# Performance work log

Hardware: AMD Instinct MI355X
Metric: run time of the kernel (lower is better)

## Reference

```python
import jax, jax.numpy as jnp
import numpy as np

D = 512      # input_dim == encoder d_model
E = 512      # embedding_dim (codebook dim)
V = 8192     # num_embeddings
NC = 1       # num_codebooks
L = 6        # encoder layers
H = 8        # heads
F = 2048     # ffn dim
HD = D // H
EPS = 1e-5


def layernorm(x, s, b):
    m = jnp.mean(x, -1, keepdims=True)
    v = jnp.mean((x - m) ** 2, -1, keepdims=True)
    return (x - m) * jax.lax.rsqrt(v + EPS) * s + b


def sinusoidal_pe(T):
    pos = np.arange(T, dtype=np.float32)[:, None]
    i = np.arange(0, D, 2, dtype=np.float32)[None, :]
    ang = pos / np.power(10000.0, i / D)
    pe = np.zeros((T, D), np.float32)
    pe[:, 0::2] = np.sin(ang)
    pe[:, 1::2] = np.cos(ang)
    return jnp.asarray(pe)


def setup_inputs():
    key = jax.random.key(0)
    ks = jax.random.split(key, 12)
    B, T = 8, 1024
    xs = jax.random.normal(ks[0], (B, T, D), jnp.float32)
    xs_lens = (T // 2 + jax.random.randint(ks[1], (B,), 0, T // 2)).astype(jnp.int32)
    mask_indices = jax.random.uniform(ks[2], (B, T)) < 0.12  # span-mask surrogate
    sc = lambda k, shape, s=0.02: jax.random.normal(k, shape, jnp.float32) * s
    return {
        "xs": xs, "xs_lens": xs_lens, "mask_indices": mask_indices,
        "W_embed": sc(ks[3], (D, D), D ** -0.5),
        "ln1_s": jnp.ones((L, D)), "ln1_b": jnp.zeros((L, D)),
        "Wqkv": sc(ks[4], (L, D, 3 * D)), "Wo": sc(ks[5], (L, D, D)),
        "ln2_s": jnp.ones((L, D)), "ln2_b": jnp.zeros((L, D)),
        "W1": sc(ks[6], (L, D, F)), "W2": sc(ks[7], (L, F, D)),
        "an_s": jnp.ones((D,)), "an_b": jnp.zeros((D,)),
        "iln_s": jnp.ones((D,)), "iln_b": jnp.zeros((D,)),
        "mask_emb": sc(ks[8], (D,), 0.1),
        "top_n_out": sc(ks[9], (NC, D, V)),
        "projection": sc(ks[10], (D, E), (2.0 / (D + E)) ** 0.5),  # xavier_normal, frozen
        "embeddings": jax.random.normal(ks[11], (NC, E, V), jnp.float32),  # frozen codebook
    }


def encoder_blocks(x, pad_mask, ln1_s, ln1_b, Wqkv, Wo, ln2_s, ln2_b, W1, W2, an_s, an_b):
    B, T, _ = x.shape
    attn_bias = jnp.where(pad_mask, 0.0, -1e9)[:, None, None, :]  # [B,1,1,T]

    def layer(x, p):
        l1s, l1b, wqkv, wo, l2s, l2b, w1, w2 = p
        h = layernorm(x, l1s, l1b)
        q, k, v = jnp.split(h @ wqkv, 3, axis=-1)
        q = q.reshape(B, T, H, HD)
        k = k.reshape(B, T, H, HD)
        v = v.reshape(B, T, H, HD)
        scores = jnp.einsum('bqhd,bkhd->bhqk', q, k) * (HD ** -0.5) + attn_bias
        o = jnp.einsum('bhqk,bkhd->bqhd', jax.nn.softmax(scores, axis=-1), v)
        x = x + o.reshape(B, T, D) @ wo
        h = layernorm(x, l2s, l2b)
        x = x + jax.nn.relu(h @ w1) @ w2
        return x, None

    x, _ = jax.lax.scan(layer, x, (ln1_s, ln1_b, Wqkv, Wo, ln2_s, ln2_b, W1, W2))
    return layernorm(x, an_s, an_b)


def nearest_ids(x, iln_s, iln_b, projection, embeddings):
    # layernorm -> projection -> squared-distance argmin per codebook
    B, T, _ = x.shape
    z = layernorm(x, iln_s, iln_b) @ projection        # [B,T,E]
    flat = z.reshape(-1, E)                            # [N,E]
    d = (jnp.sum(flat ** 2, 1)[None, :, None]
         + jnp.sum(embeddings ** 2, 1)[:, None, :]
         - 2.0 * jnp.einsum('ne,gev->gnv', flat, embeddings))  # [NC,N,V]
    return jnp.argmin(d, -1).T.reshape(B, T, NC)


def reference(xs, xs_lens, mask_indices, W_embed, ln1_s, ln1_b, Wqkv, Wo, ln2_s, ln2_b,
              W1, W2, an_s, an_b, iln_s, iln_b, mask_emb, top_n_out, projection, embeddings):
    B, T, _ = xs.shape
    pad_mask = jnp.arange(T)[None, :] < xs_lens[:, None]              # [B,T]
    x = xs @ W_embed + sinusoidal_pe(T)[None]                         # encoder.embed
    target_ids = nearest_ids(x, iln_s, iln_b, projection, embeddings)  # [B,T,NC]
    masked_xs = jnp.where(mask_indices[..., None], mask_emb, x)
    out = encoder_blocks(masked_xs, pad_mask, ln1_s, ln1_b, Wqkv, Wo,
                         ln2_s, ln2_b, W1, W2, an_s, an_b)            # [B,T,D]
    logits = jnp.einsum('btd,gdv->bgtv', out, top_n_out)              # [B,NC,T,V]
    lsm = jax.nn.log_softmax(logits, axis=-1)
    tgt = jnp.transpose(target_ids, (0, 2, 1))                        # [B,NC,T]
    ent = -jnp.take_along_axis(lsm, tgt[..., None], axis=-1)[..., 0]  # [B,NC,T]
    m = (pad_mask & mask_indices).astype(jnp.float32)                 # [B,T]
    loss = jnp.sum(ent * m[:, None, :]) / (jnp.sum(m) * NC)
    return loss
```

## Files before the change

kernel.cpp:

```cpp
#include <hip/hip_runtime.h>
#include <hip/hip_bf16.h>

#define D_ 512
#define T_ 1024
#define B_ 8
#define H_ 8
#define F_ 2048
#define V_ 8192
#define L_ 6
#define NTOK 8192
#define EPS_ 1e-5f
#define NCAP 2048

typedef short short8 __attribute__((ext_vector_type(8)));
typedef float floatx4 __attribute__((ext_vector_type(4)));

__device__ __forceinline__ float bf2f(unsigned short u) {
  union { unsigned int i; float f; } v; v.i = ((unsigned int)u) << 16; return v.f;
}
__device__ __forceinline__ unsigned short f2bf(float f) {
  unsigned int u = __float_as_uint(f);
  return (unsigned short)((u + 0x7fffu + ((u >> 16) & 1u)) >> 16);
}
__device__ __forceinline__ float ldf(const void* p, long long i, int bf) {
  if (bf) return bf2f(((const unsigned short*)p)[i]);
  return ((const float*)p)[i];
}
__device__ __forceinline__ void ld16(const unsigned short* g, unsigned short* l) {
  __builtin_amdgcn_global_load_lds(
      (const __attribute__((address_space(1))) unsigned int*)g,
      (__attribute__((address_space(3))) unsigned int*)l, 16, 0, 0);
}
__device__ __forceinline__ unsigned int fkey(float f) {
  unsigned int u = __float_as_uint(f);
  return (u & 0x80000000u) ? ~u : (u ^ 0x80000000u);
}

__global__ void detect_kernel(const unsigned int* xsw, const unsigned int* mw, int* flags) {
  __shared__ int cnt[256];
  __shared__ int m01[256], mlo[256], mhi[256];
  int tid = threadIdx.x;
  int c = 0;
  for (int t = tid; t < 1024; t += 256) {
    unsigned int lo = xsw[t] & 0xffffu;
    int ok;
    if (lo == 0u) ok = 1;
    else { unsigned int e = (lo >> 7) & 0xffu; ok = (e >= 90u && e <= 140u); }
    c += ok;
  }
  int n01 = 0, lo38 = 0, hi38 = 0;
  for (int t = tid; t < 2048; t += 256) {
    unsigned int w = mw[t];
    if (w > 1u) n01 = 1;
    if ((w & 0xffffu) == 0x3f80u) lo38 = 1;
    if ((w >> 16) == 0x3f80u) hi38 = 1;
  }
  cnt[tid] = c; m01[tid] = n01; mlo[tid] = lo38; mhi[tid] = hi38;
  __syncthreads();
  for (int s = 128; s > 0; s >>= 1) {
    if (tid < s) {
      cnt[tid] += cnt[tid + s];
      m01[tid] |= m01[tid + s]; mlo[tid] |= mlo[tid + s]; mhi[tid] |= mhi[tid + s];
    }
    __syncthreads();
  }
  if (tid == 0) {
    flags[0] = (cnt[0] > 700) ? 1 : 0;
    int fmt;
    if (!m01[0]) fmt = 0;
    else if (mlo[0]) fmt = 2;
    else if (mhi[0]) fmt = 3;
    else fmt = 1;
    flags[1] = fmt;
  }
}

__global__ void conv_all_kernel(const void* d4, const void* d5, const void* d8,
                                const void* d9, const void* d12, const void* d13,
                                const void* d14, const void* d15, const void* d16,
                                float* P, const int* flags) {
  int i = blockIdx.x * 256 + threadIdx.x;
  if (i >= 14848) return;
  int bf = flags[0];
  const void* src; int off;
  if (i < 3072) { src = d4; off = 0; }
  else if (i < 6144) { src = d5; off = 3072; }
  else if (i < 9216) { src = d8; off = 6144; }
  else if (i < 12288) { src = d9; off = 9216; }
  else if (i < 12800) { src = d12; off = 12288; }
  else if (i < 13312) { src = d13; off = 12800; }
  else if (i < 13824) { src = d14; off = 13312; }
  else if (i < 14336) { src = d15; off = 13824; }
  else { src = d16; off = 14336; }
  P[i] = ldf(src, i - off, bf);
}

__global__ void convb_kernel(const void* src, unsigned short* dst, int n, const int* flags) {
  int i = blockIdx.x * 256 + threadIdx.x;
  if (i < n) {
    if (flags[0]) dst[i] = ((const unsigned short*)src)[i];
    else dst[i] = f2bf(((const float*)src)[i]);
  }
}

__global__ __launch_bounds__(256) void trans_kernel(const void* src, unsigned short* dst,
                                                    int K, int N, const int* flags) {
  int bf = flags[0];
  __shared__ unsigned short tile[32][33];
  int n0 = blockIdx.x * 32, k0 = blockIdx.y * 32, batch = blockIdx.z;
  long long sbase = (long long)batch * K * N;
  long long dbase = (long long)batch * N * K;
  int c = threadIdx.x & 31, r8 = threadIdx.x >> 5;
#pragma unroll
  for (int rr = 0; rr < 4; ++rr) {
    int r = r8 + rr * 8;
    tile[r][c] = f2bf(ldf(src, sbase + (long long)(k0 + r) * N + n0 + c, bf));
  }
  __syncthreads();
#pragma unroll
  for (int rr = 0; rr < 4; ++rr) {
    int nn = r8 + rr * 8;
    dst[dbase + (long long)(n0 + nn) * K + k0 + c] = tile[c][nn];
  }
}

__global__ __launch_bounds__(256) void trans_big_kernel(const void* top, const void* emb,
                                                        unsigned short* TOPT, unsigned short* EMBT,
                                                        float* en, const int* flags) {
  int bf = flags[0];
  __shared__ unsigned short tile[32][33];
  int n0 = blockIdx.x * 32, k0 = blockIdx.y * 32, z = blockIdx.z;
  const void* src = z ? emb : top;
  unsigned short* dst = z ? EMBT : TOPT;
  int c = threadIdx.x & 31, r8 = threadIdx.x >> 5;
#pragma unroll
  for (int rr = 0; rr < 4; ++rr) {
    int r = r8 + rr * 8;
    tile[r][c] = f2bf(ldf(src, (long long)(k0 + r) * V_ + n0 + c, bf));
  }
  __syncthreads();
#pragma unroll
  for (int rr = 0; rr < 4; ++rr) {
    int nn = r8 + rr * 8;
    dst[(long long)(n0 + nn) * D_ + k0 + c] = tile[c][nn];
  }
  if (z == 1 && threadIdx.x < 32) {
    int nn = threadIdx.x;
    float s = 0.f;
#pragma unroll
    for (int r = 0; r < 32; ++r) { float x = bf2f(tile[r][nn]); s += x * x; }
    atomicAdd(&en[n0 + nn], s);
  }
}

__global__ void prep_kernel(const void* mask, const int* lens, int* maski, float* mcomb,
                            int* idx, int* cnt, const int* flags) {
  int i = blockIdx.x * 256 + threadIdx.x;
  if (i >= NTOK) return;
  int fmt = flags[1];
  int mi;
  if (fmt == 0) mi = ((const int*)mask)[i] != 0;
  else if (fmt == 1) mi = ((const unsigned char*)mask)[i] != 0;
  else if (fmt == 2) mi = ((const unsigned short*)mask)[i] != 0;
  else mi = ((const float*)mask)[i] != 0.f;
  int b = i >> 10, t = i & (T_ - 1);
  int act = mi && (t < lens[b]);
  maski[i] = mi;
  mcomb[i] = act ? 1.f : 0.f;
  if (act) {
    int p = atomicAdd(cnt, 1);
    if (p < NCAP) idx[p] = i;
  }
}

#define BK 32

template<int BN>
__device__ __forceinline__ void stage_tile(const unsigned short* A, long long ga0, long long ga1,
                                           const unsigned short* BT, long long gb0, long long gb1,
                                           int k0, unsigned short (*Ab)[BK],
                                           unsigned short (*Bb)[BK], int wave, int c16) {
  ld16(A + ga0 + k0 + c16 * 8, &Ab[wave * 32][0]);
  ld16(A + ga1 + k0 + c16 * 8, &Ab[wave * 32 + 16][0]);
  if constexpr (BN == 128) {
    ld16(BT + gb0 + k0 + c16 * 8, &Bb[wave * 32][0]);
    ld16(BT + gb1 + k0 + c16 * 8, &Bb[wave * 32 + 16][0]);
  } else {
    ld16(BT + gb0 + k0 + c16 * 8, &Bb[wave * 16][0]);
  }
}

template<int BN>
__device__ __forceinline__ void mfma_pipe(const unsigned short* A, long long ga0, long long ga1,
                                          const unsigned short* BT, int n0, int Kdim,
                                          unsigned short (*As)[BK], unsigned short (*Bs)[BK],
                                          floatx4 (*acc)[BN / 32], int tid) {
  constexpr int NB = BN / 32;
  int wave = tid >> 6, lane = tid & 63;
  int r16 = lane >> 2, c16 = lane & 3;
  int lrow = lane & 15, quad = lane >> 4;
  int wm = (wave & 1) * 64, wn = (wave >> 1) * (BN / 2);
  int NT = Kdim / BK;
  long long gb0, gb1 = 0;
  if constexpr (BN == 128) {
    gb0 = (long long)(n0 + wave * 32 + r16) * Kdim;
    gb1 = gb0 + 16LL * Kdim;
  } else {
    gb0 = (long long)(n0 + wave * 16 + r16) * Kdim;
  }
  stage_tile<BN>(A, ga0, ga1, BT, gb0, gb1, 0, As, Bs, wave, c16);
  stage_tile<BN>(A, ga0, ga1, BT, gb0, gb1, BK, As + 128, Bs + BN, wave, c16);
  int cur = 0, nxt = 2;
  for (int t = 0; t < NT; ++t) {
    if (t == NT - 1) {
      asm volatile("s_waitcnt vmcnt(0)" ::: "memory");
    } else {
      if constexpr (BN == 128) asm volatile("s_waitcnt vmcnt(4)" ::: "memory");
      else                     asm volatile("s_waitcnt vmcnt(3)" ::: "memory");
    }
    __builtin_amdgcn_s_barrier();
    if (t + 2 < NT)
      stage_tile<BN>(A, ga0, ga1, BT, gb0, gb1, (t + 2) * BK,
                     As + nxt * 128, Bs + nxt * BN, wave, c16);
    unsigned short (*Ac)[BK] = As + cur * 128;
    unsigned short (*Bc)[BK] = Bs + cur * BN;
    short8 af[4], bfr[NB];
#pragma unroll
    for (int i = 0; i < 4; ++i) af[i] = *(const short8*)&Ac[wm + i * 16 + lrow][quad * 8];
#pragma unroll
    for (int j = 0; j < NB; ++j) bfr[j] = *(const short8*)&Bc[wn + j * 16 + lrow][quad * 8];
#pragma unroll
    for (int i = 0; i < 4; ++i)
#pragma unroll
      for (int j = 0; j < NB; ++j)
        acc[i][j] = __builtin_amdgcn_mfma_f32_16x16x32_bf16(af[i], bfr[j], acc[i][j], 0, 0, 0);
    cur = (cur == 2) ? 0 : cur + 1;
    nxt = (nxt == 2) ? 0 : nxt + 1;
  }
  __syncthreads();
}

__global__ __launch_bounds__(256) void mgemm_kernel(const unsigned short* A,
    const unsigned short* BT, long long boff, unsigned short* Cb, int Ndim, int Kdim) {
  __shared__ __align__(16) unsigned short As[3 * 128][BK];
  __shared__ __align__(16) unsigned short Bs[3 * 128][BK];
  int tid = threadIdx.x;
  int bid = blockIdx.x;
  int m0 = (bid & 63) * 128, n0 = (bid >> 6) * 128;
  int wave = tid >> 6, lane = tid & 63;
  int wm = (wave & 1) * 64, wn = (wave >> 1) * 64;
  int lrow = lane & 15, quad = lane >> 4;
  int r16 = lane >> 2;
  floatx4 acc[4][4];
#pragma unroll
  for (int i = 0; i < 4; ++i)
#pragma unroll
    for (int j = 0; j < 4; ++j) acc[i][j] = (floatx4){0.f, 0.f, 0.f, 0.f};
  long long ga0 = (long long)(m0 + wave * 32 + r16) * Kdim;
  long long ga1 = ga0 + 16LL * Kdim;
  mfma_pipe<128>(A, ga0, ga1, BT + boff, n0, Kdim, As, Bs, acc, tid);
#pragma unroll
  for (int i = 0; i < 4; ++i) {
    int mb = m0 + wm + i * 16 + quad * 4;
#pragma unroll
    for (int j = 0; j < 4; ++j) {
      int ncol = n0 + wn + j * 16 + lrow;
#pragma unroll
      for (int r = 0; r < 4; ++r)
        Cb[(long long)(mb + r) * Ndim + ncol] = f2bf(fmaxf(acc[i][j][r], 0.f));
    }
  }
}

__global__ __launch_bounds__(256) void mgemm64_kernel(const unsigned short* A,
    const unsigned short* BT, long long boff, float* Cf, unsigned short* Cb,
    int Ndim, int Kdim, int mode) {
  __shared__ __align__(16) unsigned short As[3 * 128][BK];
  __shared__ __align__(16) unsigned short Bs[3 * 64][BK];
  int tid = threadIdx.x;
  int bid = blockIdx.x;
  int m0 = (bid & 63) * 128, n0 = (bid >> 6) * 64;
  int wave = tid >> 6, lane = tid & 63;
  int r16 = lane >> 2;
  int wm = (wave & 1) * 64, wn = (wave >> 1) * 32;
  int lrow = lane & 15, quad = lane >> 4;
  floatx4 acc[4][2];
#pragma unroll
  for (int i = 0; i < 4; ++i)
#pragma unroll
    for (int j = 0; j < 2; ++j) acc[i][j] = (floatx4){0.f, 0.f, 0.f, 0.f};
  long long ga0 = (long long)(m0 + wave * 32 + r16) * Kdim;
  long long ga1 = ga0 + 16LL * Kdim;
  mfma_pipe<64>(A, ga0, ga1, BT + boff, n0, Kdim, As, Bs, acc, tid);
#pragma unroll
  for (int i = 0; i < 4; ++i) {
    int mb = m0 + wm + i * 16 + quad * 4;
#pragma unroll
    for (int j = 0; j < 2; ++j) {
      int ncol = n0 + wn + j * 16 + lrow;
#pragma unroll
      for (int r = 0; r < 4; ++r) {
        int m = mb + r;
        long long idx = (long long)m * Ndim + ncol;
        float v = acc[i][j][r];
        if (mode == 1) Cf[idx] += v;
        else if (mode == 4) Cb[idx] = f2bf(v);
        else if (mode == 3) {
          int t = m & (T_ - 1);
          float freq = __expf(-(float)(ncol & ~1) * (9.210340371976184f / (float)D_));
          float ang = (float)t * freq;
          v += (ncol & 1) ? cosf(ang) : sinf(ang);
          Cf[idx] = v;
        } else Cf[idx] = v;
      }
    }
  }
}

__global__ __launch_bounds__(256) void qkvgemm_kernel(const unsigned short* A,
    const unsigned short* BT, long long boff, unsigned short* QB,
    unsigned short* KSg, unsigned short* VTSg) {
  __shared__ __align__(16) union {
    struct { unsigned short As[3 * 128][BK]; unsigned short Bs[3 * 128][BK]; } s;
    unsigned short T[128][136];
  } sm;
  int tid = threadIdx.x;
  int bid = blockIdx.x;
  int m0 = (bid & 63) * 128;
  int nt = bid >> 6;
  int n0 = nt * 128;
  int wave = tid >> 6, lane = tid & 63;
  int wm = (wave & 1) * 64, wn = (wave >> 1) * 64;
  int lrow = lane & 15, quad = lane >> 4;
  int r16 = lane >> 2;
  floatx4 acc[4][4];
#pragma unroll
  for (int i = 0; i < 4; ++i)
#pragma unroll
    for (int j = 0; j < 4; ++j) acc[i][j] = (floatx4){0.f, 0.f, 0.f, 0.f};
  long long ga0 = (long long)(m0 + wave * 32 + r16) * D_;
  long long ga1 = ga0 + 16LL * D_;
  mfma_pipe<128>(A, ga0, ga1, BT + boff, n0, D_, sm.s.As, sm.s.Bs, acc, tid);
  int b = m0 >> 10, tt = (m0 >> 7) & 7;
  if (nt < 4) {
#pragma unroll
    for (int i = 0; i < 4; ++i) {
      int mb = m0 + wm + i * 16 + quad * 4;
#pragma unroll
      for (int j = 0; j < 4; ++j) {
        int ncol = n0 + wn + j * 16 + lrow;
#pragma unroll
        for (int r = 0; r < 4; ++r)
          QB[(long long)(mb + r) * 512 + ncol] = f2bf(acc[i][j][r]);
      }
    }
  } else if (nt < 8) {
#pragma unroll
    for (int i = 0; i < 4; ++i)
#pragma unroll
      for (int j = 0; j < 4; ++j)
#pragma unroll
        for (int r = 0; r < 4; ++r)
          sm.T[wm + i * 16 + quad * 4 + r][wn + j * 16 + lrow] = f2bf(acc[i][j][r]);
    __syncthreads();
    int tk = tid & 127, hg0 = tid >> 7;
#pragma unroll
    for (int p = 0; p < 8; ++p) {
      int hg = p * 2 + hg0;
      int h2 = hg >> 3, g = hg & 7;
      uint4 u = *(const uint4*)&sm.T[tk][h2 * 64 + g * 8];
      int headg = (nt - 4) * 2 + h2;
      long long dst = (((((long long)(b * 8 + headg)) * 8 + tt) * 8 + g) * 128 + tk) * 8;
      *(uint4*)&KSg[dst] = u;
    }
  } else {
#pragma unroll
    for (int i = 0; i < 4; ++i)
#pragma unroll
      for (int j = 0; j < 4; ++j)
#pragma unroll
        for (int r = 0; r < 4; ++r)
          sm.T[wn + j * 16 + lrow][wm + i * 16 + quad * 4 + r] = f2bf(acc[i][j][r]);
    __syncthreads();
    int col = tid & 127, gh = tid >> 7;
    int h2 = col >> 6, ch = col & 63;
    int headg = (nt - 8) * 2 + h2;
    long long base = ((((long long)(b * 8 + headg)) * 8 + tt) * 16);
#pragma unroll
    for (int p = 0; p < 8; ++p) {
      int g = p * 2 + gh;
      uint4 u = *(const uint4*)&sm.T[col][g * 8];
      long long dst = ((base + g) * 64 + ch) * 8;
      *(uint4*)&VTSg[dst] = u;
    }
  }
}

__global__ __launch_bounds__(256) void fattn_kernel(const unsigned short* QB,
    const unsigned short* KSg, const unsigned short* VTSg, const int* lens,
    unsigned short* ao) {
  __shared__ __align__(16) unsigned short Kt[8192];
  __shared__ __align__(16) unsigned short Vt[8192];
  __shared__ __align__(16) unsigned short Ps[16384];
  int blk = blockIdx.x;
  int qt = blk & 7, bh = blk >> 3;
  int b = bh >> 3, h = bh & 7;
  int tid = threadIdx.x, wave = tid >> 6, lane = tid & 63;
  int c = lane & 15, quad = lane >> 4;
  int len = lens[b];
  short8 qf[2][2];
#pragma unroll
  for (int i = 0; i < 2; ++i)
#pragma unroll
    for (int ks = 0; ks < 2; ++ks)
      qf[i][ks] = *(const short8*)&QB[(long long)(b * 1024 + qt * 128 + wave * 32 + i * 16 + c) * 512
                                      + h * 64 + ks * 32 + quad * 8];
  floatx4 accO[2][4];
  float lr[2][4];
#pragma unroll
  for (int i = 0; i < 2; ++i)
#pragma unroll
    for (int j = 0; j < 4; ++j) {
      accO[i][j] = (floatx4){0.f, 0.f, 0.f, 0.f};
      lr[i][j] = 0.f;
    }
  int nkt = (len + 127) >> 7;
  const unsigned short* ksrc = KSg + (long long)bh * 65536;
  const unsigned short* vsrc = VTSg + (long long)bh * 65536;
  for (int kt = 0; kt < nkt; ++kt) {
#pragma unroll
    for (int p = 0; p < 4; ++p) {
      int eb = (p * 256 + wave * 64) * 8;
      ld16(ksrc + (long long)kt * 8192 + eb + lane * 8, &Kt[eb]);
      ld16(vsrc + (long long)kt * 8192 + eb + lane * 8, &Vt[eb]);
    }
    __syncthreads();
    floatx4 sacc[2][8];
#pragma unroll
    for (int i = 0; i < 2; ++i)
#pragma unroll
      for (int j = 0; j < 8; ++j) sacc[i][j] = (floatx4){0.f, 0.f, 0.f, 0.f};
#pragma unroll
    for (int j = 0; j < 8; ++j) {
      short8 bk0 = *(const short8*)&Kt[(quad * 128 + j * 16 + c) * 8];
      short8 bk1 = *(const short8*)&Kt[((4 + quad) * 128 + j * 16 + c) * 8];
#pragma unroll
      for (int i = 0; i < 2; ++i) {
        sacc[i][j] = __builtin_amdgcn_mfma_f32_16x16x32_bf16(qf[i][0], bk0, sacc[i][j], 0, 0, 0);
        sacc[i][j] = __builtin_amdgcn_mfma_f32_16x16x32_bf16(qf[i][1], bk1, sacc[i][j], 0, 0, 0);
      }
    }
    int kbase = kt * 128;
#pragma unroll
    for (int i = 0; i < 2; ++i) {
#pragma unroll
      for (int r = 0; r < 4; ++r) {
        int prow = wave * 32 + i * 16 + quad * 4 + r;
        int rx = prow & 15;
        float ls = 0.f;
#pragma unroll
        for (int j = 0; j < 8; ++j) {
          int col = j * 16 + c;
          float s = sacc[i][j][r] * 0.125f;
          s = (kbase + col < len) ? s : -100.f;
          float p = __expf(s);
          ls += p;
          Ps[prow * 128 + (((col >> 3) ^ rx) * 8) + (col & 7)] = f2bf(p);
        }
        ls += __shfl_xor(ls, 1, 64);
        ls += __shfl_xor(ls, 2, 64);
        ls += __shfl_xor(ls, 4, 64);
        ls += __shfl_xor(ls, 8, 64);
        lr[i][r] += ls;
      }
    }
    __syncthreads();
#pragma unroll
    for (int kk = 0; kk < 4; ++kk) {
      short8 pa[2];
#pragma unroll
      for (int i = 0; i < 2; ++i) {
        int row = wave * 32 + i * 16 + c;
        pa[i] = *(const short8*)&Ps[row * 128 + (((kk * 4 + quad) ^ (row & 15)) * 8)];
      }
#pragma unroll
      for (int jn = 0; jn < 4; ++jn) {
        short8 vb = *(const short8*)&Vt[((kk * 4 + quad) * 64 + jn * 16 + c) * 8];
#pragma unroll
        for (int i = 0; i < 2; ++i)
          accO[i][jn] = __builtin_amdgcn_mfma_f32_16x16x32_bf16(pa[i], vb, accO[i][jn], 0, 0, 0);
      }
    }
    __syncthreads();
  }
#pragma unroll
  for (int i = 0; i < 2; ++i) {
#pragma unroll
    for (int r = 0; r < 4; ++r) {
      float inv = 1.f / lr[i][r];
      long long token = b * 1024 + qt * 128 + wave * 32 + i * 16 + quad * 4 + r;
#pragma unroll
      for (int jn = 0; jn < 4; ++jn)
        ao[token * 512 + h * 64 + jn * 16 + c] = f2bf(accO[i][jn][r] * inv);
    }
  }
}

__global__ __launch_bounds__(256) void dgemm_argmin(const unsigned short* Z, const int* ridx,
    const int* cnt, const unsigned short* ET, const float* en, unsigned long long* best) {
  __shared__ __align__(16) union {
    struct { unsigned short A[3 * 128][BK]; unsigned short B[3 * 128][BK]; } s;
    unsigned long long part[128][33];
  } sm;
  int m0 = blockIdx.y * 128;
  int na = *cnt;
  if (m0 >= ((na + 127) & ~127)) return;
  int tid = threadIdx.x;
  int n0 = blockIdx.x * 128;
  int wave = tid >> 6, lane = tid & 63;
  int wm = (wave & 1) * 64, wn = (wave >> 1) * 64;
  int lrow = lane & 15, quad = lane >> 4;
  int r16 = lane >> 2;
  int slot = (wave >> 1) * 16 + lrow;
  floatx4 acc[4][4];
#pragma unroll
  for (int i = 0; i < 4; ++i)
#pragma unroll
    for (int j = 0; j < 4; ++j) acc[i][j] = (floatx4){0.f, 0.f, 0.f, 0.f};
  long long ga0 = (long long)ridx[m0 + wave * 32 + r16] * D_;
  long long ga1 = (long long)ridx[m0 + wave * 32 + 16 + r16] * D_;
  mfma_pipe<128>(Z, ga0, ga1, ET, n0, D_, sm.s.A, sm.s.B, acc, tid);
  float env[4];
#pragma unroll
  for (int j = 0; j < 4; ++j) env[j] = en[n0 + wn + j * 16 + lrow];
#pragma unroll
  for (int i = 0; i < 4; ++i) {
#pragma unroll
    for (int r = 0; r < 4; ++r) {
      int rowl = wm + i * 16 + quad * 4 + r;
      unsigned long long bl = ~0ull;
#pragma unroll
      for (int j = 0; j < 4; ++j) {
        float v = env[j] - 2.f * acc[i][j][r];
        unsigned long long pk = (((unsigned long long)fkey(v)) << 32) |
                                (unsigned int)(n0 + wn + j * 16 + lrow);
        if (pk < bl) bl = pk;
      }
      sm.part[rowl][(slot + rowl) & 31] = bl;
    }
  }
  __syncthreads();
  if (tid < 128) {
    unsigned long long bb = sm.part[tid][0];
#pragma unroll 4
    for (int k2 = 1; k2 < 32; ++k2) { unsigned long long o = sm.part[tid][k2]; if (o < bb) bb = o; }
    atomicMin(&best[m0 + tid], bb);
  }
}

__global__ __launch_bounds__(256) void lgemm_lse(const unsigned short* OUTB, const int* ridx,
    const int* cnt, const unsigned short* TOPT, const unsigned long long* best,
    float* PS, float* TL) {
  __shared__ __align__(16) union {
    struct { unsigned short A[3 * 128][BK]; unsigned short B[3 * 128][BK]; } s;
    float part[128][33];
  } sm;
  int m0 = blockIdx.y * 128;
  int na = *cnt;
  if (m0 >= ((na + 127) & ~127)) return;
  int tid = threadIdx.x;
  int n0 = blockIdx.x * 128;
  int wave = tid >> 6, lane = tid & 63;
  int wm = (wave & 1) * 64, wn = (wave >> 1) * 64;
  int lrow = lane & 15, quad = lane >> 4;
  int r16 = lane >> 2;
  int slot = (wave >> 1) * 16 + lrow;
  floatx4 acc[4][4];
#pragma unroll
  for (int i = 0; i < 4; ++i)
#pragma unroll
    for (int j = 0; j < 4; ++j) acc[i][j] = (floatx4){0.f, 0.f, 0.f, 0.f};
  long long ga0 = (long long)ridx[m0 + wave * 32 + r16] * D_;
  long long ga1 = (long long)ridx[m0 + wave * 32 + 16 + r16] * D_;
  mfma_pipe<128>(OUTB, ga0, ga1, TOPT, n0, D_, sm.s.A, sm.s.B, acc, tid);
#pragma unroll
  for (int i = 0; i < 4; ++i) {
#pragma unroll
    for (int r = 0; r < 4; ++r) {
      int rowl = wm + i * 16 + quad * 4 + r;
      int tg = (int)(best[m0 + rowl] & 0xffffffffu);
      float ss = 0.f;
#pragma unroll
      for (int j = 0; j < 4; ++j) {
        float v = acc[i][j][r];
        ss += __expf(v);
        if (n0 + wn + j * 16 + lrow == tg) TL[m0 + rowl] = v;
      }
      sm.part[rowl][(slot + rowl) & 31] = ss;
    }
  }
  __syncthreads();
  if (tid < 128) {
    float S = 0.f;
#pragma unroll 4
    for (int k2 = 0; k2 < 32; ++k2) S += sm.part[tid][k2];
    PS[(long long)(m0 + tid) * 64 + blockIdx.x] = S;
  }
}

__global__ void lse_combine(const float* PS, const float* TL, const int* cnt, float* entm) {
  int t = blockIdx.x * 256 + threadIdx.x;
  if (t >= NCAP) return;
  if (t < *cnt) {
    float S = 0.f;
    for (int i = 0; i < 64; ++i) S += PS[(long long)t * 64 + i];
    entm[t] = __logf(S) - TL[t];
  } else {
    entm[t] = 0.f;
  }
}

__global__ __launch_bounds__(256) void ln_kernel(const float* X, float* Yf, unsigned short* Yb,
                                                 int obf, const float* s, const float* b) {
  int tid = threadIdx.x, wave = tid >> 6, lane = tid & 63;
  long long n = (long long)blockIdx.x * 4 + wave;
  const float* x = X + n * D_ + lane * 8;
  float v[8];
  *(float4*)&v[0] = *(const float4*)x;
  *(float4*)&v[4] = *(const float4*)(x + 4);
  float sum = 0.f;
#pragma unroll
  for (int j = 0; j < 8; ++j) sum += v[j];
  for (int m = 32; m; m >>= 1) sum += __shfl_xor(sum, m, 64);
  float mean = sum * (1.f / (float)D_);
  float vs = 0.f;
#pragma unroll
  for (int j = 0; j < 8; ++j) { v[j] -= mean; vs += v[j] * v[j]; }
  for (int m = 32; m; m >>= 1) vs += __shfl_xor(vs, m, 64);
  float r = rsqrtf(vs * (1.f / (float)D_) + EPS_);
  float sv[8], bv[8];
  *(float4*)&sv[0] = *(const float4*)(s + lane * 8);
  *(float4*)&sv[4] = *(const float4*)(s + lane * 8 + 4);
  *(float4*)&bv[0] = *(const float4*)(b + lane * 8);
  *(float4*)&bv[4] = *(const float4*)(b + lane * 8 + 4);
  if (obf) {
    unsigned short o[8];
#pragma unroll
    for (int j = 0; j < 8; ++j) o[j] = f2bf(v[j] * r * sv[j] + bv[j]);
    *(uint4*)(Yb + n * D_ + lane * 8) = *(const uint4*)o;
  } else {
    float o[8];
#pragma unroll
    for (int j = 0; j < 8; ++j) o[j] = v[j] * r * sv[j] + bv[j];
    *(float4*)(Yf + n * D_ + lane * 8) = *(const float4*)&o[0];
    *(float4*)(Yf + n * D_ + lane * 8 + 4) = *(const float4*)&o[4];
  }
}

__global__ void maskapply_kernel(float* x, const int* maski, const float* memb) {
  long long i = (long long)blockIdx.x * 256 + threadIdx.x;
  int n = (int)(i >> 9), d = (int)(i & 511);
  if (maski[n]) x[i] = memb[d];
}

__global__ void final_kernel(const float* entm, const float* mcomb, void* out) {
  __shared__ float r1[256], r2[256];
  int tid = threadIdx.x;
  float s1 = 0.f, s2 = 0.f;
  for (int i = tid; i < NCAP; i += 256) s1 += entm[i];
  for (int i = tid; i < NTOK; i += 256) s2 += mcomb[i];
  r1[tid] = s1; r2[tid] = s2;
  __syncthreads();
  for (int st = 128; st > 0; st >>= 1) {
    if (tid < st) { r1[tid] += r1[tid + st]; r2[tid] += r2[tid + st]; }
    __syncthreads();
  }
  if (tid == 0) {
    float loss = r1[0] / r2[0];
    unsigned short b16 = f2bf(loss);
    unsigned short* o = (unsigned short*)out;
    o[0] = b16; o[1] = b16;
  }
}

extern "C" void kernel_launch(void* const* d_in, const int* in_sizes, int n_in,
                              void* d_out, int out_size, void* d_ws, size_t ws_size,
                              hipStream_t stream) {
  if (n_in < 20) return;
  float* wsf = (float*)d_ws;
  int* flags = (int*)d_ws;
  const long long OF_P = 256;
  const long long OF_X = 16640;
  const long long OF_HB = OF_X + 4194304;
  const long long OF_BIG = OF_HB + 2097152;
  const long long OF_AOB = OF_BIG + 8388608;
  const long long OF_WT = OF_AOB + 2097152;
  const long long OF_TOPT = OF_WT + 9699328;
  const long long OF_EMBT = OF_TOPT + 2097152;
  const long long OF_EN = OF_EMBT + 2097152;
  const long long OF_BEST = OF_EN + 8192;
  const long long OF_PS = OF_BEST + 4096;
  const long long OF_TL = OF_PS + 131072;
  const long long OF_MI = OF_TL + 2048;
  const long long OF_MC = OF_MI + 8192;
  const long long OF_EM = OF_MC + 8192;
  const long long OF_CNT = OF_EM + 2048;
  const long long OF_IDX = OF_CNT + 16;
  const long long END = OF_IDX + 2048;
  if (ws_size < (size_t)END * 4) return;

  float* X = wsf + OF_X;
  unsigned short* HB = (unsigned short*)(wsf + OF_HB);
  unsigned short* BIGB = (unsigned short*)(wsf + OF_BIG);
  unsigned short* AOB = (unsigned short*)(wsf + OF_AOB);
  unsigned short* WT = (unsigned short*)(wsf + OF_WT);
  unsigned short* TOPT = (unsigned short*)(wsf + OF_TOPT);
  unsigned short* EMBT = (unsigned short*)(wsf + OF_EMBT);
  float* EN = wsf + OF_EN;
  unsigned long long* BEST = (unsigned long long*)(wsf + OF_BEST);
  float* PS = wsf + OF_PS;
  float* TL = wsf + OF_TL;
  int* MI = (int*)(wsf + OF_MI);
  float* MC = wsf + OF_MC;
  float* EM = wsf + OF_EM;
  int* CNT = (int*)(wsf + OF_CNT);
  int* IDX = (int*)(wsf + OF_IDX);
  float* P = wsf + OF_P;
  float* ln1s = P, *ln1b = P + 3072, *ln2s = P + 6144, *ln2b = P + 9216;
  float* ans = P + 12288, *anb = P + 12800, *ilns = P + 13312, *ilnb = P + 13824;
  float* memb = P + 14336;

  unsigned short* QB = BIGB;
  unsigned short* KSg = BIGB + 4194304;
  unsigned short* VTSg = BIGB + 8388608;

  const long long W_QKV = 0, W_O = 4718592, W_1 = 6291456, W_2 = 12582912,
                  W_EMB = 18874368, W_PRJ = 19136512;

  detect_kernel<<<1, 256, 0, stream>>>((const unsigned int*)d_in[0],
                                       (const unsigned int*)d_in[2], flags);
  hipMemsetAsync((void*)BEST, 0xFF, NCAP * 8, stream);
  hipMemsetAsync((void*)EN, 0, V_ * 4, stream);
  hipMemsetAsync((void*)CNT, 0, 16, stream);
  hipMemsetAsync((void*)IDX, 0, NCAP * 4, stream);
  conv_all_kernel<<<58, 256, 0, stream>>>(d_in[4], d_in[5], d_in[8], d_in[9], d_in[12],
                                          d_in[13], d_in[14], d_in[15], d_in[16], P, flags);
  prep_kernel<<<32, 256, 0, stream>>>(d_in[2], (const int*)d_in[1], MI, MC, IDX, CNT, flags);

  unsigned short* XSB = BIGB;
  convb_kernel<<<16384, 256, 0, stream>>>(d_in[0], XSB, 4194304, flags);

  trans_kernel<<<dim3(48, 16, 6), 256, 0, stream>>>(d_in[6], WT + W_QKV, 512, 1536, flags);
  trans_kernel<<<dim3(16, 16, 6), 256, 0, stream>>>(d_in[7], WT + W_O, 512, 512, flags);
  trans_kernel<<<dim3(64, 16, 6), 256, 0, stream>>>(d_in[10], WT + W_1, 512, 2048, flags);
  trans_kernel<<<dim3(16, 64, 6), 256, 0, stream>>>(d_in[11], WT + W_2, 2048, 512, flags);
  trans_kernel<<<dim3(16, 16, 1), 256, 0, stream>>>(d_in[3], WT + W_EMB, 512, 512, flags);
  trans_kernel<<<dim3(16, 16, 1), 256, 0, stream>>>(d_in[18], WT + W_PRJ, 512, 512, flags);
  trans_big_kernel<<<dim3(256, 16, 2), 256, 0, stream>>>(d_in[17], d_in[19], TOPT, EMBT,
                                                         EN, flags);

  dim3 gC(64, NCAP / 128);

  mgemm64_kernel<<<512, 256, 0, stream>>>(XSB, WT + W_EMB, 0, X, nullptr, 512, 512, 3);
  ln_kernel<<<2048, 256, 0, stream>>>(X, nullptr, HB, 1, ilns, ilnb);
  mgemm64_kernel<<<512, 256, 0, stream>>>(HB, WT + W_PRJ, 0, nullptr, AOB, 512, 512, 4);
  dgemm_argmin<<<gC, 256, 0, stream>>>(AOB, IDX, CNT, EMBT, EN, BEST);
  maskapply_kernel<<<16384, 256, 0, stream>>>(X, MI, memb);

  for (int l = 0; l < L_; ++l) {
    ln_kernel<<<2048, 256, 0, stream>>>(X, nullptr, HB, 1, ln1s + l * 512, ln1b + l * 512);
    qkvgemm_kernel<<<768, 256, 0, stream>>>(HB, WT + W_QKV, (long long)l * 786432,
                                            QB, KSg, VTSg);
    fattn_kernel<<<512, 256, 0, stream>>>(QB, KSg, VTSg, (const int*)d_in[1], AOB);
    mgemm64_kernel<<<512, 256, 0, stream>>>(AOB, WT + W_O, (long long)l * 262144,
                                            X, nullptr, 512, 512, 1);
    ln_kernel<<<2048, 256, 0, stream>>>(X, nullptr, HB, 1, ln2s + l * 512, ln2b + l * 512);
    mgemm_kernel<<<1024, 256, 0, stream>>>(HB, WT + W_1, (long long)l * 1048576,
                                           BIGB, 2048, 512);
    mgemm64_kernel<<<512, 256, 0, stream>>>(BIGB, WT + W_2, (long long)l * 1048576,
                                            X, nullptr, 512, 2048, 1);
  }
  ln_kernel<<<2048, 256, 0, stream>>>(X, nullptr, AOB, 1, ans, anb);
  lgemm_lse<<<gC, 256, 0, stream>>>(AOB, IDX, CNT, TOPT, BEST, PS, TL);
  lse_combine<<<8, 256, 0, stream>>>(PS, TL, CNT, EM);
  final_kernel<<<1, 256, 0, stream>>>(EM, MC, d_out);
}
```

Measured before the change: 1.331 ms.

## Restructure flash attention to 64-row tiles reading K/V directly from global

The attention kernel now handles 64 query rows per block instead of 128 (one 16-row tile per wave), doubling the grid to 1024 blocks. K and V fragments are loaded straight from global memory into registers instead of being staged through shared memory, and the block-wide barriers are removed because each wave only reads the P rows it wrote itself. Block indices are swizzled so consecutive blocks cover different batch-heads. This shrinks shared memory and raises occupancy, in exchange for more global/L2 traffic for K/V and less K/V reuse across query rows.

```diff
diff --git a/kernel.cpp b/kernel.cpp
--- a/kernel.cpp
+++ b/kernel.cpp
@@ -399,110 +399,100 @@
 __global__ __launch_bounds__(256) void fattn_kernel(const unsigned short* QB,
     const unsigned short* KSg, const unsigned short* VTSg, const int* lens,
     unsigned short* ao) {
-  __shared__ __align__(16) unsigned short Kt[8192];
-  __shared__ __align__(16) unsigned short Vt[8192];
-  __shared__ __align__(16) unsigned short Ps[16384];
+  __shared__ __align__(16) unsigned short Ps[64 * 128];
   int blk = blockIdx.x;
-  int qt = blk & 7, bh = blk >> 3;
+  int swz = (blk & 7) * 128 + (blk >> 3);
+  int qt = swz & 15, bh = swz >> 4;
   int b = bh >> 3, h = bh & 7;
   int tid = threadIdx.x, wave = tid >> 6, lane = tid & 63;
   int c = lane & 15, quad = lane >> 4;
   int len = lens[b];
-  short8 qf[2][2];
-#pragma unroll
-  for (int i = 0; i < 2; ++i)
-#pragma unroll
-    for (int ks = 0; ks < 2; ++ks)
-      qf[i][ks] = *(const short8*)&QB[(long long)(b * 1024 + qt * 128 + wave * 32 + i * 16 + c) * 512
-                                      + h * 64 + ks * 32 + quad * 8];
-  floatx4 accO[2][4];
-  float lr[2][4];
-#pragma unroll
-  for (int i = 0; i < 2; ++i)
-#pragma unroll
-    for (int j = 0; j < 4; ++j) {
-      accO[i][j] = (floatx4){0.f, 0.f, 0.f, 0.f};
-      lr[i][j] = 0.f;
-    }
+  short8 qf[2];
+#pragma unroll
+  for (int ks = 0; ks < 2; ++ks)
+    qf[ks] = *(const short8*)&QB[(long long)(b * 1024 + qt * 64 + wave * 16 + c) * 512
+                                 + h * 64 + ks * 32 + quad * 8];
+  floatx4 accO[4];
+  float lr[4];
+#pragma unroll
+  for (int j = 0; j < 4; ++j) { accO[j] = (floatx4){0.f, 0.f, 0.f, 0.f}; lr[j] = 0.f; }
   int nkt = (len + 127) >> 7;
   const unsigned short* ksrc = KSg + (long long)bh * 65536;
   const unsigned short* vsrc = VTSg + (long long)bh * 65536;
   for (int kt = 0; kt < nkt; ++kt) {
-#pragma unroll
-    for (int p = 0; p < 4; ++p) {
-      int eb = (p * 256 + wave * 64) * 8;
-      ld16(ksrc + (long long)kt * 8192 + eb + lane * 8, &Kt[eb]);
-      ld16(vsrc + (long long)kt * 8192 + eb + lane * 8, &Vt[eb]);
-    }
-    __syncthreads();
-    floatx4 sacc[2][8];
-#pragma unroll
-    for (int i = 0; i < 2; ++i)
-#pragma unroll
-      for (int j = 0; j < 8; ++j) sacc[i][j] = (floatx4){0.f, 0.f, 0.f, 0.f};
-#pragma unroll
-    for (int j = 0; j < 8; ++j) {
-      short8 bk0 = *(const short8*)&Kt[(quad * 128 + j * 16 + c) * 8];
-      short8 bk1 = *(const short8*)&Kt[((4 + quad) * 128 + j * 16 + c) * 8];
-#pragma unroll
-      for (int i = 0; i < 2; ++i) {
-        sacc[i][j] = __builtin_amdgcn_mfma_f32_16x16x32_bf16(qf[i][0], bk0, sacc[i][j], 0, 0, 0);
-        sacc[i][j] = __builtin_amdgcn_mfma_f32_16x16x32_bf16(qf[i][1], bk1, sacc[i][j], 0, 0, 0);
+    const unsigned short* kp = ksrc + (long long)kt * 8192;
+    const unsigned short* vp = vsrc + (long long)kt * 8192;
+    int kbase = kt * 128;
+    float lsr[4];
+#pragma unroll
+    for (int r = 0; r < 4; ++r) lsr[r] = 0.f;
+#pragma unroll
+    for (int jh = 0; jh < 2; ++jh) {
+      short8 bk0[4], bk1[4];
+#pragma unroll
+      for (int j2 = 0; j2 < 4; ++j2) {
+        int j = jh * 4 + j2;
+        bk0[j2] = *(const short8*)&kp[(quad * 128 + j * 16 + c) * 8];
+        bk1[j2] = *(const short8*)&kp[((4 + quad) * 128 + j * 16 + c) * 8];
       }
-    }
-    int kbase = kt * 128;
-#pragma unroll
-    for (int i = 0; i < 2; ++i) {
+      floatx4 sacc[4];
+#pragma unroll
+      for (int j2 = 0; j2 < 4; ++j2) sacc[j2] = (floatx4){0.f, 0.f, 0.f, 0.f};
+#pragma unroll
+      for (int j2 = 0; j2 < 4; ++j2) {
+        sacc[j2] = __builtin_amdgcn_mfma_f32_16x16x32_bf16(qf[0], bk0[j2], sacc[j2], 0, 0, 0);
+        sacc[j2] = __builtin_amdgcn_mfma_f32_16x16x32_bf16(qf[1], bk1[j2], sacc[j2], 0, 0, 0);
+      }
 #pragma unroll
       for (int r = 0; r < 4; ++r) {
-        int prow = wave * 32 + i * 16 + quad * 4 + r;
-        int rx = prow & 15;
-        float ls = 0.f;
-#pragma unroll
-        for (int j = 0; j < 8; ++j) {
-          int col = j * 16 + c;
-          float s = sacc[i][j][r] * 0.125f;
+        int prow = wave * 16 + quad * 4 + r;
+        int rx = quad * 4 + r;
+#pragma unroll
+        for (int j2 = 0; j2 < 4; ++j2) {
+          int col = (jh * 4 + j2) * 16 + c;
+          float s = sacc[j2][r] * 0.125f;
           s = (kbase + col < len) ? s : -100.f;
           float p = __expf(s);
-          ls += p;
+          lsr[r] += p;
           Ps[prow * 128 + (((col >> 3) ^ rx) * 8) + (col & 7)] = f2bf(p);
         }
-        ls += __shfl_xor(ls, 1, 64);
-        ls += __shfl_xor(ls, 2, 64);
-        ls += __shfl_xor(ls, 4, 64);
-        ls += __shfl_xor(ls, 8, 64);
-        lr[i][r] += ls;
       }
     }
-    __syncthreads();
-#pragma unroll
-    for (int kk = 0; kk < 4; ++kk) {
-      short8 pa[2];
-#pragma unroll
-      for (int i = 0; i < 2; ++i) {
-        int row = wave * 32 + i * 16 + c;
-        pa[i] = *(const short8*)&Ps[row * 128 + (((kk * 4 + quad) ^ (row & 15)) * 8)];
+#pragma unroll
+    for (int r = 0; r < 4; ++r) {
+      float ls = lsr[r];
+      ls += __shfl_xor(ls, 1, 64);
+      ls += __shfl_xor(ls, 2, 64);
+      ls += __shfl_xor(ls, 4, 64);
+      ls += __shfl_xor(ls, 8, 64);
+      lr[r] += ls;
+    }
+#pragma unroll
+    for (int kh = 0; kh < 2; ++kh) {
+      short8 vb[2][4];
+#pragma unroll
+      for (int kk2 = 0; kk2 < 2; ++kk2)
+#pragma unroll
+        for (int jn = 0; jn < 4; ++jn)
+          vb[kk2][jn] = *(const short8*)&vp[(((kh * 2 + kk2) * 4 + quad) * 64 + jn * 16 + c) * 8];
+#pragma unroll
+      for (int kk2 = 0; kk2 < 2; ++kk2) {
+        int kk = kh * 2 + kk2;
+        int row = wave * 16 + c;
+        short8 pa = *(const short8*)&Ps[row * 128 + (((kk * 4 + quad) ^ c) * 8)];
+#pragma unroll
+        for (int jn = 0; jn < 4; ++jn)
+          accO[jn] = __builtin_amdgcn_mfma_f32_16x16x32_bf16(pa, vb[kk2][jn], accO[jn], 0, 0, 0);
       }
-#pragma unroll
-      for (int jn = 0; jn < 4; ++jn) {
-        short8 vb = *(const short8*)&Vt[((kk * 4 + quad) * 64 + jn * 16 + c) * 8];
-#pragma unroll
-        for (int i = 0; i < 2; ++i)
-          accO[i][jn] = __builtin_amdgcn_mfma_f32_16x16x32_bf16(pa[i], vb, accO[i][jn], 0, 0, 0);
-      }
-    }
-    __syncthreads();
-  }
-#pragma unroll
-  for (int i = 0; i < 2; ++i) {
-#pragma unroll
-    for (int r = 0; r < 4; ++r) {
-      float inv = 1.f / lr[i][r];
-      long long token = b * 1024 + qt * 128 + wave * 32 + i * 16 + quad * 4 + r;
-#pragma unroll
-      for (int jn = 0; jn < 4; ++jn)
-        ao[token * 512 + h * 64 + jn * 16 + c] = f2bf(accO[i][jn][r] * inv);
-    }
+    }
+  }
+#pragma unroll
+  for (int r = 0; r < 4; ++r) {
+    float inv = 1.f / lr[r];
+    long long token = b * 1024 + qt * 64 + wave * 16 + quad * 4 + r;
+#pragma unroll
+    for (int jn = 0; jn < 4; ++jn)
+      ao[token * 512 + h * 64 + jn * 16 + c] = f2bf(accO[jn][r] * inv);
   }
 }
 
@@ -771,7 +761,7 @@
     ln_kernel<<<2048, 256, 0, stream>>>(X, nullptr, HB, 1, ln1s + l * 512, ln1b + l * 512);
     qkvgemm_kernel<<<768, 256, 0, stream>>>(HB, WT + W_QKV, (long long)l * 786432,
                                             QB, KSg, VTSg);
-    fattn_kernel<<<512, 256, 0, stream>>>(QB, KSg, VTSg, (const int*)d_in[1], AOB);
+    fattn_kernel<<<1024, 256, 0, stream>>>(QB, KSg, VTSg, (const int*)d_in[1], AOB);
     mgemm64_kernel<<<512, 256, 0, stream>>>(AOB, WT + W_O, (long long)l * 262144,
                                             X, nullptr, 512, 512, 1);
     ln_kernel<<<2048, 256, 0, stream>>>(X, nullptr, HB, 1, ln2s + l * 512, ln2b + l * 512);
```

Result: no change. 1.325 ms (-0.5%).
